# Optimization experiments

Measured on AMD Instinct MI355X. Metric: run time of the kernel, lower is better.

The kernel has to match this reference:

```python
import jax, jax.numpy as jnp
import numpy as np

DT = 1.0
V_LAMBDA = 1e-4
V_RIDGE = 1e-4


def third_order_D(Np):
    # [Np-3, Np] banded third-difference operator
    M = Np - 3
    r = jnp.arange(M)
    D = jnp.zeros((M, Np), dtype=jnp.float32)
    D = D.at[r, r].set(-1.0).at[r, r + 1].set(3.0).at[r, r + 2].set(-3.0).at[r, r + 3].set(1.0)
    return D


def setup_inputs() -> dict:
    key = jax.random.key(0)
    k1, k2, k3 = jax.random.split(key, 3)
    B, N = 8192, 64
    dxy = jax.random.normal(k1, (B, N, 2), dtype=jnp.float32)
    theta = jax.random.normal(k2, (B, N + 1), dtype=jnp.float32)
    v0 = jax.random.normal(k3, (B,), dtype=jnp.float32)
    return {"dxy": dxy, "theta": theta, "v0": v0}


def reference(dxy, theta, v0):
    B, N, _ = dxy.shape  # theta: [B, N+1]
    g = (2.0 / DT) * dxy                     # [B, N, 2]
    b = g.reshape(B, 2 * N)                  # interleaved (x, y) per step
    cos_t = jnp.cos(theta)
    sin_t = jnp.sin(theta)

    # Assemble banded data matrix A: [B, 2N, N+1]
    rows = jnp.arange(N)
    A = jnp.zeros((B, 2 * N, N + 1), dtype=dxy.dtype)
    A = A.at[:, 2 * rows, rows].set(cos_t[:, :-1])
    A = A.at[:, 2 * rows, rows + 1].set(cos_t[:, 1:])
    A = A.at[:, 2 * rows + 1, rows].set(sin_t[:, :-1])
    A = A.at[:, 2 * rows + 1, rows + 1].set(sin_t[:, 1:])
    # data weights w = 1 -> Aw == A

    ATA = jnp.einsum('bij,bik->bjk', A, A)           # [B, N+1, N+1]
    rhs = jnp.einsum('bij,bi->bj', A[:, :, 1:], b)   # [B, N]
    rhs = rhs - ATA[:, 1:, 0] * v0[:, None]

    # Smoothness prior: third-order difference, lam3 = v_lambda / dt^6
    D3 = third_order_D(N + 1)
    DTD = (V_LAMBDA / DT ** 6) * (D3.T @ D3)         # [N+1, N+1], shared across batch
    rhs = rhs - DTD[1:, 0] * v0[:, None]

    lhs = ATA[:, 1:, 1:] + DTD[1:, 1:] + V_RIDGE * jnp.eye(N, dtype=dxy.dtype)
    L = jnp.linalg.cholesky(lhs)
    y = jax.scipy.linalg.cho_solve((L, True), rhs[..., None])[..., 0]  # [B, N]
    return jnp.concatenate([v0[:, None], y], axis=-1)                  # [B, N+1]
```

## Files before the change

### kernel.cpp

```cpp
#include <hip/hip_runtime.h>
#include <math.h>

#define LAM3  1e-4f
#define RIDGE 1e-4f
#define NN    64
#define NP    65

__device__ __forceinline__ float d3_diag(int f) {
    if (f == 0 || f == 64) return 1.f;
    if (f == 1 || f == 63) return 10.f;
    if (f == 2 || f == 62) return 19.f;
    return 20.f;
}
__device__ __forceinline__ float d3_off1(int f) {
    if (f == 1 || f == 64) return -3.f;
    if (f == 2 || f == 63) return -12.f;
    return -15.f;
}
__device__ __forceinline__ float d3_off2(int f) {
    if (f == 2 || f == 64) return 3.f;
    return 6.f;
}

__global__ __launch_bounds__(256, 1) void alpamayo_prep(
    const float* __restrict__ dxy,
    const float* __restrict__ theta,
    const float* __restrict__ v0,
    float* __restrict__ eT,
    float* __restrict__ rT,
    int B)
{
    __shared__ __attribute__((aligned(16))) float thS[64 * NP];
    __shared__ float cS[64 * NP];
    __shared__ float sS[64 * NP];
    __shared__ float bxS[64 * NP];
    __shared__ float byS[64 * NP];

    const int tid = threadIdx.x;
    const int b0 = blockIdx.x * 64;

    {
        const float4* g = (const float4*)(theta + (long)b0 * NP);
        float4* s4 = (float4*)thS;
        #pragma unroll
        for (int it = 0; it < 5; ++it) {
            const int k = it * 256 + tid;
            if (k < 1040) s4[k] = g[k];
        }
    }
    {
        const float4* g = (const float4*)(dxy + (long)b0 * 128);
        #pragma unroll
        for (int it = 0; it < 8; ++it) {
            const int k = it * 256 + tid;
            const float4 q = g[k];
            const int flat = 4 * k;
            const int bl = flat >> 7;
            const int i  = (flat & 127) >> 1;
            float* bx = bxS + bl * NP + i;
            float* by = byS + bl * NP + i;
            bx[0] = q.x; by[0] = q.y; bx[1] = q.z; by[1] = q.w;
        }
    }
    if (tid < 64) { bxS[tid * NP + 64] = 0.f; byS[tid * NP + 64] = 0.f; }
    __syncthreads();

    #pragma unroll
    for (int it = 0; it < 17; ++it) {
        const int k = it * 256 + tid;
        if (k < 4160) {
            float sv, cv;
            __sincosf(thS[k], &sv, &cv);
            sS[k] = sv; cS[k] = cv;
        }
    }
    __syncthreads();

    const int bl = tid & 63;
    const int qr = tid >> 6;
    const int b  = b0 + bl;
    const float* cL  = cS  + bl * NP;
    const float* sL  = sS  + bl * NP;
    const float* bxL = bxS + bl * NP;
    const float* byL = byS + bl * NP;
    const float v0b = v0[b];

    #pragma unroll
    for (int p = 0; p < 16; ++p) {
        const int i = p * 4 + qr;
        const int f = i + 1;
        const float e   = cL[i] * cL[f] + sL[i] * sL[f];
        float rhs = 2.f * (cL[f] * (bxL[i] + bxL[f]) + sL[f] * (byL[i] + byL[f]));
        if (i == 0) rhs -= (e + LAM3 * -3.f) * v0b;
        if (i == 1) rhs -= (LAM3 *  3.f) * v0b;
        if (i == 2) rhs -= (LAM3 * -1.f) * v0b;
        eT[i * B + b] = e;
        rT[i * B + b] = rhs;
    }
}

__global__ __launch_bounds__(64, 1) void alpamayo_solve(
    const float* __restrict__ eT,
    const float* __restrict__ rT,
    const float* __restrict__ v0,
    float* __restrict__ out,
    int B)
{
    __shared__ __attribute__((aligned(16))) float yS[64 * NP];

    const int tid = threadIdx.x;
    const int b0 = blockIdx.x * 64;
    const int b  = b0 + tid;

    float L1a[NN], L2a[NN], L3a[NN], rda[NN], z[NN];

    float p1L1 = 0.f, p1L2 = 0.f, p2L1 = 0.f;
    float rd1 = 0.f, rd2 = 0.f, rd3 = 0.f;
    float z1 = 0.f, z2 = 0.f, z3 = 0.f;

    const float* ep = eT + b;
    const float* rp = rT + b;

    #pragma unroll
    for (int i = 0; i < NN; ++i) {
        const int f = i + 1;
        const float e   = ep[i * B];
        const float rhs = rp[i * B];

        const float a0 = (f == NN ? 1.f : 2.f) + LAM3 * d3_diag(f) + RIDGE;
        const float a1 = e + LAM3 * d3_off1(f);
        const float a2 = LAM3 * d3_off2(f);
        const float a3 = LAM3 * -1.f;

        const float Li3 = a3 * rd3;
        const float Li2 = (a2 - Li3 * p2L1) * rd2;
        const float Li1 = (a1 - Li3 * p1L2 - Li2 * p1L1) * rd1;
        const float dg  = a0 - Li3 * Li3 - Li2 * Li2 - Li1 * Li1;
        const float rd0 = __builtin_amdgcn_rsqf(dg);
        const float zi  = (rhs - Li3 * z3 - Li2 * z2 - Li1 * z1) * rd0;

        L1a[i] = Li1; L2a[i] = Li2; L3a[i] = Li3; rda[i] = rd0; z[i] = zi;

        p2L1 = p1L1; p1L1 = Li1; p1L2 = Li2;
        rd3 = rd2; rd2 = rd1; rd1 = rd0;
        z3 = z2; z2 = z1; z1 = zi;
    }

    float* yL = yS + tid * NP;
    float y1 = 0.f, y2 = 0.f, y3 = 0.f;
    #pragma unroll
    for (int i = NN - 1; i >= 0; --i) {
        float yi = z[i];
        if (i + 1 < NN) yi -= L1a[i + 1] * y1;
        if (i + 2 < NN) yi -= L2a[i + 2] * y2;
        if (i + 3 < NN) yi -= L3a[i + 3] * y3;
        yi *= rda[i];
        yL[1 + i] = yi;
        y3 = y2; y2 = y1; y1 = yi;
    }
    yL[0] = v0[b];
    __syncthreads();

    float4* go = (float4*)(out + (long)b0 * NP);
    const float4* s4 = (const float4*)yS;
    #pragma unroll
    for (int it = 0; it < 17; ++it) {
        const int k = it * 64 + tid;
        if (k < 1040) go[k] = s4[k];
    }
}

extern "C" void kernel_launch(void* const* d_in, const int* in_sizes, int n_in,
                              void* d_out, int out_size, void* d_ws, size_t ws_size,
                              hipStream_t stream) {
    const float* dxy   = (const float*)d_in[0];
    const float* theta = (const float*)d_in[1];
    const float* v0    = (const float*)d_in[2];
    float* out = (float*)d_out;
    const int B = in_sizes[2];

    float* eT = (float*)d_ws;
    float* rT = eT + (long)NN * B;

    const int blocks = (B + 63) / 64;
    alpamayo_prep <<<blocks, 256, 0, stream>>>(dxy, theta, v0, eT, rT, B);
    alpamayo_solve<<<blocks,  64, 0, stream>>>(eT, rT, v0, out, B);
}
```

Measured before the change: 68.30 us.

## Fuse prep and banded Cholesky solve into one kernel via LDS

```diff
diff --git a/kernel.cpp b/kernel.cpp
--- a/kernel.cpp
+++ b/kernel.cpp
@@ -22,19 +22,19 @@
     return 6.f;
 }
 
-__global__ __launch_bounds__(256, 1) void alpamayo_prep(
+__global__ __launch_bounds__(256, 1) void alpamayo_fused(
     const float* __restrict__ dxy,
     const float* __restrict__ theta,
     const float* __restrict__ v0,
-    float* __restrict__ eT,
-    float* __restrict__ rT,
+    float* __restrict__ out,
     int B)
 {
     __shared__ __attribute__((aligned(16))) float thS[64 * NP];
-    __shared__ float cS[64 * NP];
-    __shared__ float sS[64 * NP];
     __shared__ float bxS[64 * NP];
     __shared__ float byS[64 * NP];
+    __shared__ float eS[NN * 64];
+    __shared__ float rS[NN * 64];
+    __shared__ __attribute__((aligned(16))) float4 L4[NN][64];
 
     const int tid = threadIdx.x;
     const int b0 = blockIdx.x * 64;
@@ -62,111 +62,103 @@
             bx[0] = q.x; by[0] = q.y; bx[1] = q.z; by[1] = q.w;
         }
     }
-    if (tid < 64) { bxS[tid * NP + 64] = 0.f; byS[tid * NP + 64] = 0.f; }
+    float v0b = 0.f;
+    if (tid < 64) {
+        bxS[tid * NP + 64] = 0.f;
+        byS[tid * NP + 64] = 0.f;
+        v0b = v0[b0 + tid];
+    }
     __syncthreads();
 
-    #pragma unroll
-    for (int it = 0; it < 17; ++it) {
-        const int k = it * 256 + tid;
-        if (k < 4160) {
-            float sv, cv;
-            __sincosf(thS[k], &sv, &cv);
-            sS[k] = sv; cS[k] = cv;
+    {
+        const int bl = tid & 63;
+        const int q  = tid >> 6;
+        const int fb = q * 16;
+        const float* thL = thS + bl * NP;
+        const float* bxL = bxS + bl * NP;
+        const float* byL = byS + bl * NP;
+
+        float cc[17], ss[17];
+        #pragma unroll
+        for (int j = 0; j < 17; ++j) __sincosf(thL[fb + j], &ss[j], &cc[j]);
+
+        const float vq = (q == 0) ? v0b : 0.f;
+        #pragma unroll
+        for (int p = 0; p < 16; ++p) {
+            const int i = fb + p;
+            const int f = i + 1;
+            const float e = cc[p] * cc[p + 1] + ss[p] * ss[p + 1];
+            float rhs = 2.f * (cc[p + 1] * (bxL[i] + bxL[f]) +
+                               ss[p + 1] * (byL[i] + byL[f]));
+            if (q == 0) {
+                if (p == 0) rhs -= (e + LAM3 * -3.f) * vq;
+                if (p == 1) rhs -= (LAM3 *  3.f) * vq;
+                if (p == 2) rhs -= (LAM3 * -1.f) * vq;
+            }
+            eS[i * 64 + bl] = e;
+            rS[i * 64 + bl] = rhs;
         }
     }
     __syncthreads();
 
-    const int bl = tid & 63;
-    const int qr = tid >> 6;
-    const int b  = b0 + bl;
-    const float* cL  = cS  + bl * NP;
-    const float* sL  = sS  + bl * NP;
-    const float* bxL = bxS + bl * NP;
-    const float* byL = byS + bl * NP;
-    const float v0b = v0[b];
+    if (tid < 64) {
+        float z[NN];
+        float p1L1 = 0.f, p1L2 = 0.f, p2L1 = 0.f;
+        float rd1 = 0.f, rd2 = 0.f, rd3 = 0.f;
+        float z1 = 0.f, z2 = 0.f, z3 = 0.f;
 
-    #pragma unroll
-    for (int p = 0; p < 16; ++p) {
-        const int i = p * 4 + qr;
-        const int f = i + 1;
-        const float e   = cL[i] * cL[f] + sL[i] * sL[f];
-        float rhs = 2.f * (cL[f] * (bxL[i] + bxL[f]) + sL[f] * (byL[i] + byL[f]));
-        if (i == 0) rhs -= (e + LAM3 * -3.f) * v0b;
-        if (i == 1) rhs -= (LAM3 *  3.f) * v0b;
-        if (i == 2) rhs -= (LAM3 * -1.f) * v0b;
-        eT[i * B + b] = e;
-        rT[i * B + b] = rhs;
+        #pragma unroll
+        for (int i = 0; i < NN; ++i) {
+            const int f = i + 1;
+            const float e   = eS[i * 64 + tid];
+            const float rhs = rS[i * 64 + tid];
+
+            const float a0 = (f == NN ? 1.f : 2.f) + LAM3 * d3_diag(f) + RIDGE;
+            const float a1 = e + LAM3 * d3_off1(f);
+            const float a2 = LAM3 * d3_off2(f);
+            const float a3 = LAM3 * -1.f;
+
+            const float Li3 = a3 * rd3;
+            const float Li2 = (a2 - Li3 * p2L1) * rd2;
+            const float Li1 = (a1 - Li3 * p1L2 - Li2 * p1L1) * rd1;
+            const float dg  = a0 - Li3 * Li3 - Li2 * Li2 - Li1 * Li1;
+            const float rd0 = __builtin_amdgcn_rsqf(dg);
+            const float zi  = (rhs - Li3 * z3 - Li2 * z2 - Li1 * z1) * rd0;
+
+            L4[i][tid] = make_float4(Li1, Li2, Li3, rd0);
+            z[i] = zi;
+
+            p2L1 = p1L1; p1L1 = Li1; p1L2 = Li2;
+            rd3 = rd2; rd2 = rd1; rd1 = rd0;
+            z3 = z2; z2 = z1; z1 = zi;
+        }
+
+        float* yL = thS + tid * NP;
+        float r1L1 = 0.f, r1L2 = 0.f, r1L3 = 0.f;
+        float r2L2 = 0.f, r2L3 = 0.f;
+        float r3L3 = 0.f;
+        float y1 = 0.f, y2 = 0.f, y3 = 0.f;
+        #pragma unroll
+        for (int i = NN - 1; i >= 0; --i) {
+            const float4 rec = L4[i][tid];
+            const float yi = (z[i] - r1L1 * y1 - r2L2 * y2 - r3L3 * y3) * rec.w;
+            yL[1 + i] = yi;
+            r3L3 = r2L3; r2L3 = r1L3; r2L2 = r1L2;
+            r1L1 = rec.x; r1L2 = rec.y; r1L3 = rec.z;
+            y3 = y2; y2 = y1; y1 = yi;
+        }
+        yL[0] = v0b;
     }
-}
-
-__global__ __launch_bounds__(64, 1) void alpamayo_solve(
-    const float* __restrict__ eT,
-    const float* __restrict__ rT,
-    const float* __restrict__ v0,
-    float* __restrict__ out,
-    int B)
-{
-    __shared__ __attribute__((aligned(16))) float yS[64 * NP];
-
-    const int tid = threadIdx.x;
-    const int b0 = blockIdx.x * 64;
-    const int b  = b0 + tid;
-
-    float L1a[NN], L2a[NN], L3a[NN], rda[NN], z[NN];
-
-    float p1L1 = 0.f, p1L2 = 0.f, p2L1 = 0.f;
-    float rd1 = 0.f, rd2 = 0.f, rd3 = 0.f;
-    float z1 = 0.f, z2 = 0.f, z3 = 0.f;
-
-    const float* ep = eT + b;
-    const float* rp = rT + b;
-
-    #pragma unroll
-    for (int i = 0; i < NN; ++i) {
-        const int f = i + 1;
-        const float e   = ep[i * B];
-        const float rhs = rp[i * B];
-
-        const float a0 = (f == NN ? 1.f : 2.f) + LAM3 * d3_diag(f) + RIDGE;
-        const float a1 = e + LAM3 * d3_off1(f);
-        const float a2 = LAM3 * d3_off2(f);
-        const float a3 = LAM3 * -1.f;
-
-        const float Li3 = a3 * rd3;
-        const float Li2 = (a2 - Li3 * p2L1) * rd2;
-        const float Li1 = (a1 - Li3 * p1L2 - Li2 * p1L1) * rd1;
-        const float dg  = a0 - Li3 * Li3 - Li2 * Li2 - Li1 * Li1;
-        const float rd0 = __builtin_amdgcn_rsqf(dg);
-        const float zi  = (rhs - Li3 * z3 - Li2 * z2 - Li1 * z1) * rd0;
-
-        L1a[i] = Li1; L2a[i] = Li2; L3a[i] = Li3; rda[i] = rd0; z[i] = zi;
-
-        p2L1 = p1L1; p1L1 = Li1; p1L2 = Li2;
-        rd3 = rd2; rd2 = rd1; rd1 = rd0;
-        z3 = z2; z2 = z1; z1 = zi;
-    }
-
-    float* yL = yS + tid * NP;
-    float y1 = 0.f, y2 = 0.f, y3 = 0.f;
-    #pragma unroll
-    for (int i = NN - 1; i >= 0; --i) {
-        float yi = z[i];
-        if (i + 1 < NN) yi -= L1a[i + 1] * y1;
-        if (i + 2 < NN) yi -= L2a[i + 2] * y2;
-        if (i + 3 < NN) yi -= L3a[i + 3] * y3;
-        yi *= rda[i];
-        yL[1 + i] = yi;
-        y3 = y2; y2 = y1; y1 = yi;
-    }
-    yL[0] = v0[b];
     __syncthreads();
 
-    float4* go = (float4*)(out + (long)b0 * NP);
-    const float4* s4 = (const float4*)yS;
-    #pragma unroll
-    for (int it = 0; it < 17; ++it) {
-        const int k = it * 64 + tid;
-        if (k < 1040) go[k] = s4[k];
+    {
+        float4* g = (float4*)(out + (long)b0 * NP);
+        const float4* s4 = (const float4*)thS;
+        #pragma unroll
+        for (int it = 0; it < 5; ++it) {
+            const int k = it * 256 + tid;
+            if (k < 1040) g[k] = s4[k];
+        }
     }
 }
 
@@ -178,11 +170,6 @@
     const float* v0    = (const float*)d_in[2];
     float* out = (float*)d_out;
     const int B = in_sizes[2];
-
-    float* eT = (float*)d_ws;
-    float* rT = eT + (long)NN * B;
-
-    const int blocks = (B + 63) / 64;
-    alpamayo_prep <<<blocks, 256, 0, stream>>>(dxy, theta, v0, eT, rT, B);
-    alpamayo_solve<<<blocks,  64, 0, stream>>>(eT, rT, v0, out, B);
+    const int blocks = B / 64;
+    alpamayo_fused<<<blocks, 256, 0, stream>>>(dxy, theta, v0, out, B);
 }
```

After: 65.11 us. 1.05x faster.
